# Kernel optimization log

Hardware: AMD Instinct MI355X
Metric: run time of the kernel (lower is better)

The kernel has to match this reference:

```python
import jax, jax.numpy as jnp
import numpy as np

NGRAM = 3  # no_repeat_ngram_size from init_kwargs


def setup_inputs() -> dict:
    key = jax.random.key(0)
    k1, k2 = jax.random.split(key)
    B = 64 * 8          # bsz * beam_size
    L = 512             # step + 1 tokens generated so far
    V = 50257           # vocab
    tokens = jax.random.randint(k1, (B, L), 0, 50, dtype=jnp.int64)
    lprobs = jax.random.normal(k2, (B, V), dtype=jnp.float32)
    return {"tokens": tokens, "lprobs": lprobs, "bsz": 64, "beam_size": 8, "step": 511}


def _ngram_block(tokens, lprobs, step, n):
    """Vectorized equivalent of NGramRepeatBlock._no_repeat_ngram.

    For each row, the last n-1 tokens form the ngram prefix; any earlier
    position i in [0, step+2-n) whose (n-1)-gram matches it bans the token
    that followed it (tokens[i + n - 1]).
    """
    B, L = tokens.shape
    check = step + 2 - n  # number of start positions to check (static)
    if check <= 0:
        return lprobs
    # sliding (n-1)-gram windows at starts 0..check-1: (B, check, n-1)
    win_idx = jnp.arange(check)[:, None] + jnp.arange(n - 1)[None, :]
    windows = tokens[:, win_idx]
    prefix = tokens[:, L - (n - 1):]                    # (B, n-1) last n-1 tokens
    match = jnp.all(windows == prefix[:, None, :], -1)  # (B, check)
    banned_ids = tokens[:, n - 1: n - 1 + check]        # token following each window
    rows = jnp.arange(B)[:, None]
    banned = jnp.zeros(lprobs.shape, bool).at[rows, banned_ids].max(match)
    return jnp.where(banned, -jnp.inf, lprobs)


def reference(tokens, lprobs, bsz, beam_size, step):
    assert tokens.shape[0] == bsz * beam_size
    assert lprobs.shape[0] == bsz * beam_size
    return _ngram_block(tokens, lprobs, step, NGRAM)
```

## Files before the change

kernel.cpp:

```cpp
#include <hip/hip_runtime.h>

#define NGRAM 3

#define BAN_VALUE (-1.0e30f)

__global__ void copy_f4_kernel(const float* __restrict__ in,
                               float* __restrict__ out, long long n) {
    long long idx = (long long)blockIdx.x * blockDim.x + threadIdx.x;
    long long i4 = idx * 4;
    if (i4 + 3 < n) {
        float4 v = *(const float4*)(in + i4);
        *(float4*)(out + i4) = v;
    } else if (i4 < n) {
        for (long long j = i4; j < n; ++j) out[j] = in[j];
    }
}

__global__ void ban_kernel(const int* __restrict__ tokens,
                           float* __restrict__ out,
                           const int* __restrict__ step_p,
                           int L, int V) {
    const int row = blockIdx.x;
    const int step = *step_p;
    const int check = step + 2 - NGRAM;
    if (check <= 0) return;

    const int* t = tokens + (long long)row * L;
    const int p0 = t[L - 2];
    const int p1 = t[L - 1];
    float* orow = out + (long long)row * V;

    for (int i = threadIdx.x; i < check; i += blockDim.x) {
        if (t[i] == p0 && t[i + 1] == p1) {
            orow[t[i + 2]] = BAN_VALUE;
        }
    }
}

extern "C" void kernel_launch(void* const* d_in, const int* in_sizes, int n_in,
                              void* d_out, int out_size, void* d_ws, size_t ws_size,
                              hipStream_t stream) {
    const int*   tokens = (const int*)d_in[0];
    const float* lprobs = (const float*)d_in[1];
    const int*   step_p = (const int*)d_in[4];
    float*       out    = (float*)d_out;

    const int L = 512;
    const int B = in_sizes[0] / L;
    const int V = in_sizes[1] / B;
    const long long n = (long long)in_sizes[1];

    const long long n4 = (n + 3) / 4;
    const int threads = 256;
    const int blocksA = (int)((n4 + threads - 1) / threads);
    copy_f4_kernel<<<blocksA, threads, 0, stream>>>(lprobs, out, n);

    ban_kernel<<<B, threads, 0, stream>>>(tokens, out, step_p, L, V);
}
```

Before: 187.6 us.

## Fuse lprobs copy and n-gram ban into a single chunked kernel

Replaces the separate vectorized copy kernel and per-row ban kernel with one kernel. Each block handles a 1024-float chunk: it loads the chunk with nontemporal loads, scans the token rows overlapping that chunk to build a shared-memory ban bitmask, then applies the mask and writes with nontemporal stores. This removes one launch and the second pass of scattered writes into the output. In exchange, every block re-reads its row's token history, adding redundant L2 traffic and compute per chunk.

Result: no change. 191.3 us (+2.0%).

```diff
diff --git a/kernel.cpp b/kernel.cpp
--- a/kernel.cpp
+++ b/kernel.cpp
@@ -1,38 +1,71 @@
 #include <hip/hip_runtime.h>
 
 #define NGRAM 3
+#define BAN_VALUE (-1.0e30f)
+#define CHUNK 1024
 
-#define BAN_VALUE (-1.0e30f)
+typedef float f32x4 __attribute__((ext_vector_type(4)));
 
-__global__ void copy_f4_kernel(const float* __restrict__ in,
-                               float* __restrict__ out, long long n) {
-    long long idx = (long long)blockIdx.x * blockDim.x + threadIdx.x;
-    long long i4 = idx * 4;
-    if (i4 + 3 < n) {
-        float4 v = *(const float4*)(in + i4);
-        *(float4*)(out + i4) = v;
-    } else if (i4 < n) {
-        for (long long j = i4; j < n; ++j) out[j] = in[j];
-    }
-}
+__global__ void __launch_bounds__(256)
+fused_copy_ban(const float* __restrict__ lprobs,
+               const int* __restrict__ tokens,
+               float* __restrict__ out,
+               const int* __restrict__ step_p,
+               int L, int V, long long n) {
+    __shared__ unsigned mask[CHUNK / 32];
 
-__global__ void ban_kernel(const int* __restrict__ tokens,
-                           float* __restrict__ out,
-                           const int* __restrict__ step_p,
-                           int L, int V) {
-    const int row = blockIdx.x;
+    const int tid = threadIdx.x;
+    const long long base = (long long)blockIdx.x * CHUNK;
+    if (tid < CHUNK / 32) mask[tid] = 0u;
+
     const int step = *step_p;
     const int check = step + 2 - NGRAM;
-    if (check <= 0) return;
 
-    const int* t = tokens + (long long)row * L;
-    const int p0 = t[L - 2];
-    const int p1 = t[L - 1];
-    float* orow = out + (long long)row * V;
+    long long end = base + CHUNK;
+    if (end > n) end = n;
+    const int r0 = (int)(base / V);
+    const int r1 = (int)((end - 1) / V);
 
-    for (int i = threadIdx.x; i < check; i += blockDim.x) {
-        if (t[i] == p0 && t[i + 1] == p1) {
-            orow[t[i + 2]] = BAN_VALUE;
+    const long long i4 = base + 4LL * tid;
+    f32x4 v;
+    bool full = (i4 + 3 < n);
+    if (full) v = __builtin_nontemporal_load((const f32x4*)(lprobs + i4));
+
+    __syncthreads();
+
+    if (check > 0) {
+        for (int r = r0; r <= r1; ++r) {
+            const int* t = tokens + (long long)r * L;
+            const int p0 = t[L - 2];
+            const int p1 = t[L - 1];
+            const long long rowbase = (long long)r * V;
+            for (int i = tid; i < check; i += 256) {
+                if (t[i] == p0 && t[i + 1] == p1) {
+                    const long long g = rowbase + t[i + 2];
+                    if (g >= base && g < end) {
+                        const int local = (int)(g - base);
+                        atomicOr(&mask[local >> 5], 1u << (local & 31));
+                    }
+                }
+            }
+        }
+    }
+    __syncthreads();
+
+    if (full) {
+        const unsigned w = mask[tid >> 3];
+        const int sh = (tid & 7) * 4;
+        if (w & (1u << (sh + 0))) v.x = BAN_VALUE;
+        if (w & (1u << (sh + 1))) v.y = BAN_VALUE;
+        if (w & (1u << (sh + 2))) v.z = BAN_VALUE;
+        if (w & (1u << (sh + 3))) v.w = BAN_VALUE;
+        __builtin_nontemporal_store(v, (f32x4*)(out + i4));
+    } else if (i4 < n) {
+        for (long long j = i4; j < n; ++j) {
+            const int local = (int)(j - base);
+            float s = lprobs[j];
+            if (mask[local >> 5] & (1u << (local & 31))) s = BAN_VALUE;
+            out[j] = s;
         }
     }
 }
@@ -50,10 +83,6 @@
     const int V = in_sizes[1] / B;
     const long long n = (long long)in_sizes[1];
 
-    const long long n4 = (n + 3) / 4;
-    const int threads = 256;
-    const int blocksA = (int)((n4 + threads - 1) / threads);
-    copy_f4_kernel<<<blocksA, threads, 0, stream>>>(lprobs, out, n);
-
-    ban_kernel<<<B, threads, 0, stream>>>(tokens, out, step_p, L, V);
+    const int blocks = (int)((n + CHUNK - 1) / CHUNK);
+    fused_copy_ban<<<blocks, 256, 0, stream>>>(lprobs, tokens, out, step_p, L, V, n);
 }
```
